# Kernel tuning notes

Measured on AMD Instinct MI355X. Metric: run time of the kernel, lower is better.

Reference implementation:

```python
import jax, jax.numpy as jnp
import numpy as np
import math

RES_SCALE = 1.0
NEG_INF = -1e20
NORM_EPS = 5e-5


def _conv(x, w, pad):
    return jax.lax.conv_general_dilated(
        x, w, window_strides=(1, 1), padding=((pad, pad), (pad, pad)),
        dimension_numbers=("NCHW", "OIHW", "NCHW"))


def _blockify(t, bH, bW, nH, nW):
    # [N,C,H,W] -> [N, block_size, n_blocks, C]  (matches torch Unfold with
    # kernel=(bH,bW), stride=(bH,bW) then reshape+permute(0,2,3,1))
    n, c, _, _ = t.shape
    t = t.reshape(n, c, nH, bH, nW, bW)
    t = t.transpose(0, 1, 3, 5, 2, 4)          # [N,C,bH,bW,nH,nW]
    t = t.reshape(n, c, bH * bW, nH * nW)
    return t.transpose(0, 2, 3, 1)             # [N, block, n_blk, C]


def _unblockify(t, bH, bW, nH, nW):
    # [N, block_size, n_blocks, C] -> [N,C,H,W] (torch Fold inverse)
    n, blk, nblk, c = t.shape
    t = t.transpose(0, 3, 1, 2)                # [N,C,block,n_blk]
    t = t.reshape(n, c, bH, bW, nH, nW)
    t = t.transpose(0, 1, 4, 2, 5, 3)          # [N,C,nH,bH,nW,bW]
    return t.reshape(n, c, nH * bH, nW * bW)


def setup_inputs() -> dict:
    key = jax.random.key(0)
    k1, k2, k3, k4, k5 = jax.random.split(key, 5)
    N, C, H, W = 8, 64, 256, 256
    Cq = C // 4  # reduction=4
    x = jax.random.normal(k1, (N, C, H, W), dtype=jnp.float32)
    w_match = jax.random.normal(k2, (Cq, C, 3, 3), dtype=jnp.float32) * (1.0 / math.sqrt(C * 9))
    b_match = jax.random.normal(k3, (Cq,), dtype=jnp.float32) * 0.01
    w_asm = jax.random.normal(k4, (C, C, 1, 1), dtype=jnp.float32) * (1.0 / math.sqrt(C))
    b_asm = jax.random.normal(k5, (C,), dtype=jnp.float32) * 0.01
    return {"x": x, "w_match": w_match, "b_match": b_match,
            "w_asm": w_asm, "b_asm": b_asm}


def reference(x, w_match, b_match, w_asm, b_asm):
    N, C, H, W = x.shape
    bH = math.ceil(math.sqrt(H)); nH = bH
    bW = math.ceil(math.sqrt(W)); nW = bW
    # H=W=256 -> bH=bW=16, perfect blocking, no padding needed.
    block_size = bH * bW
    n_blocks = nH * nW

    x_embed = _conv(x, w_match, pad=1) + b_match[None, :, None, None]   # [N,Cq,H,W]
    y_embed = _conv(x, w_asm, pad=0) + b_asm[None, :, None, None]       # [N,C,H,W]

    xq = _blockify(x_embed, bH, bW, nH, nW)   # [N, block, n_blk, Cq]
    yv = _blockify(y_embed, bH, bW, nH, nW)   # [N, block, n_blk, C]

    # F.normalize(p=2, dim=-1, eps=5e-5): x / max(||x||, eps)
    norm = jnp.sqrt(jnp.sum(xq * xq, axis=-1, keepdims=True))
    xk = xq / jnp.maximum(norm, NORM_EPS)

    # attention across blocks at fixed intra-block position
    raw = jnp.einsum("bkie,bkje->bkij", xq, xk)      # [N, block, n_blk, n_blk]
    diag = jnp.eye(n_blocks, dtype=bool)
    raw = jnp.where(diag[None, None], NEG_INF, raw)
    score = jax.nn.softmax(raw, axis=-1)             # exp(raw - logsumexp)

    ret = jnp.einsum("bkij,bkje->bkie", score, yv)   # [N, block, n_blk, C]
    ret = _unblockify(ret, bH, bW, nH, nW)           # [N,C,H,W]

    return ret * RES_SCALE + x
```

## Files before the change

kernel.cpp:

```cpp
#include <hip/hip_runtime.h>
#include <math.h>

typedef __attribute__((ext_vector_type(8))) short bf16x8;
typedef __attribute__((ext_vector_type(4))) float f32x4;

#define HH 256
#define WW 256
#define HW (HH*WW)
#define NORM_EPS 5e-5f

#define OFF_WASMT   0
#define OFF_WMATT   4096
#define OFF_RNORM   16384
#define OFF_QBLK    540672
#define OFF_VBLK    8929280

__global__ void k_transpose_w(const float* __restrict__ w_asm,
                              const float* __restrict__ w_match,
                              float* __restrict__ ws) {
    int t = threadIdx.x;
    float* wasmT = ws + OFF_WASMT;
    float* wmatT = ws + OFF_WMATT;
    for (int idx = t; idx < 64 * 64; idx += 256) {
        int ci = idx >> 6, c = idx & 63;
        wasmT[ci * 64 + c] = w_asm[c * 64 + ci];
    }
    for (int idx = t; idx < 576 * 16; idx += 256) {
        int e = idx & 15, r = idx >> 4;
        wmatT[idx] = w_match[e * 576 + r];
    }
}

__global__ __launch_bounds__(256) void k_conv1x1(const float* __restrict__ x,
                                                 const float* __restrict__ b_asm,
                                                 const float* __restrict__ ws_r,
                                                 float* __restrict__ vblk) {
    int p = blockIdx.x * 256 + threadIdx.x;
    int n = p >> 16;
    int h = (p >> 8) & 255;
    int w = p & 255;
    const float* wasmT = ws_r + OFF_WASMT;

    float acc[64];
#pragma unroll
    for (int c = 0; c < 64; ++c) acc[c] = b_asm[c];

    const float* xp = x + n * (64 * HW) + h * WW + w;
#pragma unroll 4
    for (int ci = 0; ci < 64; ++ci) {
        float xv = xp[ci * HW];
        const float* wr = wasmT + ci * 64;
#pragma unroll
        for (int c = 0; c < 64; ++c) acc[c] = fmaf(xv, wr[c], acc[c]);
    }

    int k = ((h & 15) << 4) | (w & 15);
    int j = ((h >> 4) << 4) | (w >> 4);
    float* out = vblk + (size_t)(((n << 8) | k) * 256 + j) * 64;
#pragma unroll
    for (int c4 = 0; c4 < 16; ++c4) {
        reinterpret_cast<float4*>(out)[c4] =
            make_float4(acc[c4 * 4], acc[c4 * 4 + 1], acc[c4 * 4 + 2], acc[c4 * 4 + 3]);
    }
}

__global__ __launch_bounds__(256) void k_conv3x3(const float* __restrict__ x,
                                                 const float* __restrict__ b_match,
                                                 const float* __restrict__ ws_r,
                                                 float* __restrict__ qblk,
                                                 float* __restrict__ rnorm) {
    int p = blockIdx.x * 256 + threadIdx.x;
    int n = p >> 16;
    int h = (p >> 8) & 255;
    int w = p & 255;
    const float* wmatT = ws_r + OFF_WMATT;

    float acc[16];
#pragma unroll
    for (int e = 0; e < 16; ++e) acc[e] = b_match[e];

    const float* xb = x + n * (64 * HW) + h * WW + w;
    bool hm = h > 0, hp = h < 255, wmk = w > 0, wpk = w < 255;

    for (int ci = 0; ci < 64; ++ci) {
        const float* xc = xb + ci * HW;
        float xv[9];
        xv[0] = (hm && wmk) ? xc[-WW - 1] : 0.f;
        xv[1] = hm          ? xc[-WW]     : 0.f;
        xv[2] = (hm && wpk) ? xc[-WW + 1] : 0.f;
        xv[3] = wmk         ? xc[-1]      : 0.f;
        xv[4] =               xc[0];
        xv[5] = wpk         ? xc[1]       : 0.f;
        xv[6] = (hp && wmk) ? xc[WW - 1]  : 0.f;
        xv[7] = hp          ? xc[WW]      : 0.f;
        xv[8] = (hp && wpk) ? xc[WW + 1]  : 0.f;
        const float* wr = wmatT + ci * 144;
#pragma unroll
        for (int t9 = 0; t9 < 9; ++t9) {
            float v = xv[t9];
#pragma unroll
            for (int e = 0; e < 16; ++e) acc[e] = fmaf(v, wr[t9 * 16 + e], acc[e]);
        }
    }

    float ss = 0.f;
#pragma unroll
    for (int e = 0; e < 16; ++e) ss = fmaf(acc[e], acc[e], ss);
    float rn = 1.0f / fmaxf(sqrtf(ss), NORM_EPS);

    int k = ((h & 15) << 4) | (w & 15);
    int j = ((h >> 4) << 4) | (w >> 4);
    size_t base = (size_t)(((n << 8) | k) * 256 + j);
    rnorm[base] = rn;
    float* out = qblk + base * 16;
#pragma unroll
    for (int e4 = 0; e4 < 4; ++e4) {
        reinterpret_cast<float4*>(out)[e4] =
            make_float4(acc[e4 * 4], acc[e4 * 4 + 1], acc[e4 * 4 + 2], acc[e4 * 4 + 3]);
    }
}

#define QP  0
#define KP  20480
#define VTH 40960
#define VTL 50176
#define PB  59392

#define MFMA16(A,B,C) __builtin_amdgcn_mfma_f32_16x16x32_bf16((A),(B),(C),0,0,0)

__global__ __launch_bounds__(256, 2) void k_attn(const float* __restrict__ ws_r,
                                                 float* __restrict__ vblk) {
    __shared__ __align__(16) unsigned char sm[64512];
    const int tid  = threadIdx.x;
    const int lane = tid & 63;
    const int wv   = tid >> 6;
    const int g    = lane >> 4;
    const int l15  = lane & 15;
    const bool hi32 = lane >= 32;
    const int b = blockIdx.x;

    const bf16x8 zfrag = {0,0,0,0,0,0,0,0};

    const float* qbase  = ws_r + OFF_QBLK  + (size_t)b * (256 * 16);
    const float* rnbase = ws_r + OFF_RNORM + (size_t)b * 256;
    float* vbase = vblk + (size_t)b * (256 * 64);

    {
        const int t = tid;
        float rn = rnbase[t];
        const float4* q4 = reinterpret_cast<const float4*>(qbase + t * 16);
        float q[16];
#pragma unroll
        for (int r = 0; r < 4; ++r) {
            float4 v = q4[r];
            q[4*r+0] = v.x; q[4*r+1] = v.y; q[4*r+2] = v.z; q[4*r+3] = v.w;
        }
        unsigned qh[8], ql[8], kh[8], kl[8];
#pragma unroll
        for (int e = 0; e < 8; ++e) {
            float a0 = q[2*e], a1 = q[2*e+1];
            unsigned u0 = __float_as_uint(a0) & 0xFFFF0000u;
            unsigned u1 = __float_as_uint(a1) & 0xFFFF0000u;
            float r0 = a0 - __uint_as_float(u0);
            float r1 = a1 - __uint_as_float(u1);
            qh[e] = (u0 >> 16) | u1;
            ql[e] = ((__float_as_uint(r0) & 0xFFFF0000u) >> 16) | (__float_as_uint(r1) & 0xFFFF0000u);
            float k0 = a0 * rn, k1 = a1 * rn;
            unsigned v0 = __float_as_uint(k0) & 0xFFFF0000u;
            unsigned v1 = __float_as_uint(k1) & 0xFFFF0000u;
            float s0 = k0 - __uint_as_float(v0);
            float s1 = k1 - __uint_as_float(v1);
            kh[e] = (v0 >> 16) | v1;
            kl[e] = ((__float_as_uint(s0) & 0xFFFF0000u) >> 16) | (__float_as_uint(s1) & 0xFFFF0000u);
        }
        uint4* qrow = reinterpret_cast<uint4*>(sm + QP + t * 80);
        qrow[0] = make_uint4(qh[0], qh[1], qh[2], qh[3]);
        qrow[1] = make_uint4(qh[4], qh[5], qh[6], qh[7]);
        qrow[2] = make_uint4(ql[0], ql[1], ql[2], ql[3]);
        qrow[3] = make_uint4(ql[4], ql[5], ql[6], ql[7]);
        uint4* krow = reinterpret_cast<uint4*>(sm + KP + t * 80);
        krow[0] = make_uint4(kh[0], kh[1], kh[2], kh[3]);
        krow[1] = make_uint4(kh[4], kh[5], kh[6], kh[7]);
        krow[2] = make_uint4(kl[0], kl[1], kl[2], kl[3]);
        krow[3] = make_uint4(kl[4], kl[5], kl[6], kl[7]);
    }
    __syncthreads();

    bf16x8 qb1[4], qb2[4];
#pragma unroll
    for (int it = 0; it < 4; ++it) {
        int i0 = wv * 64 + it * 16;
        qb1[it] = *reinterpret_cast<const bf16x8*>(sm + QP + (i0 + l15) * 80 + (g & 1) * 16);
        bf16x8 t2 = *reinterpret_cast<const bf16x8*>(sm + QP + (i0 + l15) * 80 + 32 + (g & 1) * 16);
        qb2[it] = hi32 ? zfrag : t2;
    }

    float mrow[4] = {-1e30f, -1e30f, -1e30f, -1e30f};
    for (int jt = 0; jt < 16; ++jt) {
        bf16x8 kf = *reinterpret_cast<const bf16x8*>(sm + KP + (jt * 16 + l15) * 80 + g * 16);
#pragma unroll
        for (int it = 0; it < 4; ++it) {
            f32x4 s = {0.f, 0.f, 0.f, 0.f};
            s = MFMA16(kf, qb1[it], s);
            s = MFMA16(kf, qb2[it], s);
            bool dtile = (jt * 16 == wv * 64 + it * 16);
#pragma unroll
            for (int r = 0; r < 4; ++r) {
                float v = s[r];
                if (dtile && (4 * g + r == l15)) v = -1e30f;
                mrow[it] = fmaxf(mrow[it], v);
            }
        }
    }
#pragma unroll
    for (int it = 0; it < 4; ++it) {
        float m = mrow[it];
        m = fmaxf(m, __shfl_xor(m, 16, 64));
        m = fmaxf(m, __shfl_xor(m, 32, 64));
        mrow[it] = m;
    }

    float lsum[4] = {0.f, 0.f, 0.f, 0.f};
    f32x4 acc[4][4];
#pragma unroll
    for (int it = 0; it < 4; ++it)
#pragma unroll
        for (int ct = 0; ct < 4; ++ct) acc[it][ct] = (f32x4){0.f, 0.f, 0.f, 0.f};

    for (int ch = 0; ch < 4; ++ch) {
        __syncthreads();
        {
            int c = tid >> 2, jq = tid & 3;
            const float* vg = vbase + (size_t)(ch * 64) * 64 + c;
#pragma unroll
            for (int s2 = 0; s2 < 8; ++s2) {
                int jl = jq * 16 + s2 * 2;
                float v0 = vg[(size_t)jl * 64];
                float v1 = vg[(size_t)(jl + 1) * 64];
                unsigned u0 = __float_as_uint(v0) & 0xFFFF0000u;
                unsigned u1 = __float_as_uint(v1) & 0xFFFF0000u;
                float r0 = v0 - __uint_as_float(u0);
                float r1 = v1 - __uint_as_float(u1);
                *reinterpret_cast<unsigned*>(sm + VTH + c * 144 + jl * 2) = (u0 >> 16) | u1;
                *reinterpret_cast<unsigned*>(sm + VTL + c * 144 + jl * 2) =
                    ((__float_as_uint(r0) & 0xFFFF0000u) >> 16) | (__float_as_uint(r1) & 0xFFFF0000u);
            }
        }
        __syncthreads();

#pragma unroll
        for (int jt = 0; jt < 4; ++jt) {
            int jg0 = ch * 64 + jt * 16;
            int jl0 = jt * 16;
            bf16x8 kf = *reinterpret_cast<const bf16x8*>(sm + KP + (jg0 + l15) * 80 + g * 16);
            bf16x8 vh[4], vl[4];
#pragma unroll
            for (int ct = 0; ct < 4; ++ct) {
                vh[ct] = *reinterpret_cast<const bf16x8*>(
                    sm + VTH + (ct * 16 + l15) * 144 + (jl0 + 8 * (g & 1)) * 2);
                bf16x8 t2 = *reinterpret_cast<const bf16x8*>(
                    sm + VTL + (ct * 16 + l15) * 144 + (jl0 + 8 * (g & 1)) * 2);
                vl[ct] = hi32 ? zfrag : t2;
            }
#pragma unroll
            for (int it = 0; it < 4; ++it) {
                f32x4 s = {0.f, 0.f, 0.f, 0.f};
                s = MFMA16(kf, qb1[it], s);
                s = MFMA16(kf, qb2[it], s);
                bool dtile = (jg0 == wv * 64 + it * 16);
                unsigned pd[4];
#pragma unroll
                for (int r = 0; r < 4; ++r) {
                    float p = __expf(s[r] - mrow[it]);
                    if (dtile && (4 * g + r == l15)) p = 0.f;
                    lsum[it] += p;
                    unsigned uh = __float_as_uint(p) & 0xFFFF0000u;
                    float lo = p - __uint_as_float(uh);
                    unsigned ul = __float_as_uint(lo) & 0xFFFF0000u;
                    pd[r] = (uh >> 16) | ul;
                }
                *reinterpret_cast<uint4*>(sm + PB + wv * 1280 + l15 * 80 + g * 16) =
                    make_uint4(pd[0], pd[1], pd[2], pd[3]);
                const uint4 d0 = *reinterpret_cast<const uint4*>(sm + PB + wv * 1280 + l15 * 80 + (g & 1) * 32);
                const uint4 d1 = *reinterpret_cast<const uint4*>(sm + PB + wv * 1280 + l15 * 80 + (g & 1) * 32 + 16);
                unsigned bw0, bw1, bw2, bw3;
                if (!hi32) {
                    bw0 = (d0.x & 0xFFFFu) | (d0.y << 16);
                    bw1 = (d0.z & 0xFFFFu) | (d0.w << 16);
                    bw2 = (d1.x & 0xFFFFu) | (d1.y << 16);
                    bw3 = (d1.z & 0xFFFFu) | (d1.w << 16);
                } else {
                    bw0 = (d0.x >> 16) | (d0.y & 0xFFFF0000u);
                    bw1 = (d0.z >> 16) | (d0.w & 0xFFFF0000u);
                    bw2 = (d1.x >> 16) | (d1.y & 0xFFFF0000u);
                    bw3 = (d1.z >> 16) | (d1.w & 0xFFFF0000u);
                }
                union { uint4 u; bf16x8 s8; } pb_u;
                pb_u.u = make_uint4(bw0, bw1, bw2, bw3);
                bf16x8 pb = pb_u.s8;
#pragma unroll
                for (int ct = 0; ct < 4; ++ct) {
                    acc[it][ct] = MFMA16(vh[ct], pb, acc[it][ct]);
                    acc[it][ct] = MFMA16(vl[ct], pb, acc[it][ct]);
                }
            }
        }
    }

#pragma unroll
    for (int it = 0; it < 4; ++it) {
        float l = lsum[it];
        l += __shfl_xor(l, 16, 64);
        l += __shfl_xor(l, 32, 64);
        lsum[it] = 1.0f / l;
    }

    __syncthreads();
    const int obase = VTH + wv * 4352;
#pragma unroll
    for (int it = 0; it < 4; ++it) {
#pragma unroll
        for (int ct = 0; ct < 4; ++ct) {
#pragma unroll
            for (int r = 0; r < 4; ++r) {
                int c = ct * 16 + 4 * g + r;
                *reinterpret_cast<float*>(sm + obase + l15 * 272 + c * 4) =
                    acc[it][ct][r] * lsum[it];
            }
        }
        int ir = lane >> 2, cq = lane & 3;
        float* orow = vbase + (size_t)(wv * 64 + it * 16 + ir) * 64 + cq * 16;
#pragma unroll
        for (int k4 = 0; k4 < 4; ++k4) {
            float4 ov = *reinterpret_cast<const float4*>(sm + obase + ir * 272 + cq * 64 + k4 * 16);
            reinterpret_cast<float4*>(orow)[k4] = ov;
        }
    }
}

__global__ __launch_bounds__(256) void k_unblock(const float* __restrict__ oblk,
                                                 const float* __restrict__ x,
                                                 float* __restrict__ out) {
    int b = blockIdx.x;
    int n = b >> 8, h = b & 255;
    int t = threadIdx.x;
    int c = t & 63, wq = t >> 6;
    int kh = h & 15, jh = h >> 4;

    const float* ob = oblk + ((size_t)n << 22);
    size_t xoff = (((size_t)(n * 64 + c)) << 16) + ((size_t)h << 8);
    const float4* xr   = reinterpret_cast<const float4*>(x + xoff);
    float4*       outr = reinterpret_cast<float4*>(out + xoff);

    for (int it = 0; it < 16; ++it) {
        int w4 = wq * 16 + it;
        int w0 = w4 * 4;
        float vals[4];
#pragma unroll
        for (int r = 0; r < 4; ++r) {
            int w = w0 + r;
            int wm = w & 15, wd = w >> 4;
            vals[r] = ob[(((size_t)(kh * 16 + wm)) << 14) + ((jh * 16 + wd) << 6) + c];
        }
        float4 xv = xr[w4];
        outr[w4] = make_float4(vals[0] + xv.x, vals[1] + xv.y, vals[2] + xv.z, vals[3] + xv.w);
    }
}

extern "C" void kernel_launch(void* const* d_in, const int* in_sizes, int n_in,
                              void* d_out, int out_size, void* d_ws, size_t ws_size,
                              hipStream_t stream) {
    const float* x       = (const float*)d_in[0];
    const float* w_match = (const float*)d_in[1];
    const float* b_match = (const float*)d_in[2];
    const float* w_asm   = (const float*)d_in[3];
    const float* b_asm   = (const float*)d_in[4];
    float* out = (float*)d_out;
    float* ws  = (float*)d_ws;

    k_transpose_w<<<1, 256, 0, stream>>>(w_asm, w_match, ws);
    k_conv1x1<<<2048, 256, 0, stream>>>(x, b_asm, ws, ws + OFF_VBLK);
    k_conv3x3<<<2048, 256, 0, stream>>>(x, b_match, ws, ws + OFF_QBLK, ws + OFF_RNORM);
    k_attn<<<2048, 256, 0, stream>>>(ws, ws + OFF_VBLK);
    k_unblock<<<2048, 256, 0, stream>>>(ws + OFF_VBLK, x, out);
}
```

Baseline: 704.1 us.

## Fuse 1x1 and 3x3 convs into one MFMA kernel with split-bf16 precision

Replaces the two scalar-FMA convolution kernels with a single fused kernel that stages three input rows, with halo, in shared memory as hi/lo bf16 pairs. Both convolutions then run as bf16 MFMA GEMMs, using three products (hh, lh, hl) to approximate fp32 accuracy. The goal is to cut the heavy scalar FMA cost and read x only once for both convs. The risks are precision loss from dropping the lo*lo term and scattered 4-byte global stores into the blocked layout.

```diff
diff --git a/kernel.cpp b/kernel.cpp
--- a/kernel.cpp
+++ b/kernel.cpp
@@ -9,114 +9,180 @@
 #define HW (HH*WW)
 #define NORM_EPS 5e-5f
 
-#define OFF_WASMT   0
-#define OFF_WMATT   4096
+#define MFMA16(A,B,C) __builtin_amdgcn_mfma_f32_16x16x32_bf16((A),(B),(C),0,0,0)
+
 #define OFF_RNORM   16384
 #define OFF_QBLK    540672
 #define OFF_VBLK    8929280
-
-__global__ void k_transpose_w(const float* __restrict__ w_asm,
-                              const float* __restrict__ w_match,
-                              float* __restrict__ ws) {
+#define WASMH_U 0
+#define WASML_U 4096
+#define WMATH_U 8192
+#define WMATL_U 17408
+
+__global__ void k_prep(const float* __restrict__ w_asm,
+                       const float* __restrict__ w_match,
+                       unsigned short* __restrict__ wsu) {
     int t = threadIdx.x;
-    float* wasmT = ws + OFF_WASMT;
-    float* wmatT = ws + OFF_WMATT;
-    for (int idx = t; idx < 64 * 64; idx += 256) {
-        int ci = idx >> 6, c = idx & 63;
-        wasmT[ci * 64 + c] = w_asm[c * 64 + ci];
-    }
-    for (int idx = t; idx < 576 * 16; idx += 256) {
-        int e = idx & 15, r = idx >> 4;
-        wmatT[idx] = w_match[e * 576 + r];
+    for (int i = t; i < 4096; i += 256) {
+        float v = w_asm[i];
+        unsigned hh = __float_as_uint(v) & 0xFFFF0000u;
+        float lo = v - __uint_as_float(hh);
+        wsu[WASMH_U + i] = (unsigned short)(hh >> 16);
+        wsu[WASML_U + i] = (unsigned short)(__float_as_uint(lo) >> 16);
+    }
+    for (int i = t; i < 9216; i += 256) {
+        int tap = i >> 10, cout = (i >> 6) & 15, ci = i & 63;
+        float v = w_match[(cout * 64 + ci) * 9 + tap];
+        unsigned hh = __float_as_uint(v) & 0xFFFF0000u;
+        float lo = v - __uint_as_float(hh);
+        wsu[WMATH_U + i] = (unsigned short)(hh >> 16);
+        wsu[WMATL_U + i] = (unsigned short)(__float_as_uint(lo) >> 16);
     }
 }
 
-__global__ __launch_bounds__(256) void k_conv1x1(const float* __restrict__ x,
-                                                 const float* __restrict__ b_asm,
-                                                 const float* __restrict__ ws_r,
-                                                 float* __restrict__ vblk) {
-    int p = blockIdx.x * 256 + threadIdx.x;
-    int n = p >> 16;
-    int h = (p >> 8) & 255;
-    int w = p & 255;
-    const float* wasmT = ws_r + OFF_WASMT;
-
-    float acc[64];
-#pragma unroll
-    for (int c = 0; c < 64; ++c) acc[c] = b_asm[c];
-
-    const float* xp = x + n * (64 * HW) + h * WW + w;
-#pragma unroll 4
-    for (int ci = 0; ci < 64; ++ci) {
-        float xv = xp[ci * HW];
-        const float* wr = wasmT + ci * 64;
-#pragma unroll
-        for (int c = 0; c < 64; ++c) acc[c] = fmaf(xv, wr[c], acc[c]);
-    }
-
-    int k = ((h & 15) << 4) | (w & 15);
-    int j = ((h >> 4) << 4) | (w >> 4);
-    float* out = vblk + (size_t)(((n << 8) | k) * 256 + j) * 64;
-#pragma unroll
-    for (int c4 = 0; c4 < 16; ++c4) {
-        reinterpret_cast<float4*>(out)[c4] =
-            make_float4(acc[c4 * 4], acc[c4 * 4 + 1], acc[c4 * 4 + 2], acc[c4 * 4 + 3]);
-    }
-}
-
-__global__ __launch_bounds__(256) void k_conv3x3(const float* __restrict__ x,
-                                                 const float* __restrict__ b_match,
-                                                 const float* __restrict__ ws_r,
-                                                 float* __restrict__ qblk,
-                                                 float* __restrict__ rnorm) {
-    int p = blockIdx.x * 256 + threadIdx.x;
-    int n = p >> 16;
-    int h = (p >> 8) & 255;
-    int w = p & 255;
-    const float* wmatT = ws_r + OFF_WMATT;
-
-    float acc[16];
-#pragma unroll
-    for (int e = 0; e < 16; ++e) acc[e] = b_match[e];
-
-    const float* xb = x + n * (64 * HW) + h * WW + w;
-    bool hm = h > 0, hp = h < 255, wmk = w > 0, wpk = w < 255;
-
-    for (int ci = 0; ci < 64; ++ci) {
-        const float* xc = xb + ci * HW;
-        float xv[9];
-        xv[0] = (hm && wmk) ? xc[-WW - 1] : 0.f;
-        xv[1] = hm          ? xc[-WW]     : 0.f;
-        xv[2] = (hm && wpk) ? xc[-WW + 1] : 0.f;
-        xv[3] = wmk         ? xc[-1]      : 0.f;
-        xv[4] =               xc[0];
-        xv[5] = wpk         ? xc[1]       : 0.f;
-        xv[6] = (hp && wmk) ? xc[WW - 1]  : 0.f;
-        xv[7] = hp          ? xc[WW]      : 0.f;
-        xv[8] = (hp && wpk) ? xc[WW + 1]  : 0.f;
-        const float* wr = wmatT + ci * 144;
-#pragma unroll
-        for (int t9 = 0; t9 < 9; ++t9) {
-            float v = xv[t9];
-#pragma unroll
-            for (int e = 0; e < 16; ++e) acc[e] = fmaf(v, wr[t9 * 16 + e], acc[e]);
-        }
-    }
-
-    float ss = 0.f;
-#pragma unroll
-    for (int e = 0; e < 16; ++e) ss = fmaf(acc[e], acc[e], ss);
-    float rn = 1.0f / fmaxf(sqrtf(ss), NORM_EPS);
-
-    int k = ((h & 15) << 4) | (w & 15);
-    int j = ((h >> 4) << 4) | (w >> 4);
-    size_t base = (size_t)(((n << 8) | k) * 256 + j);
-    rnorm[base] = rn;
-    float* out = qblk + base * 16;
-#pragma unroll
-    for (int e4 = 0; e4 < 4; ++e4) {
-        reinterpret_cast<float4*>(out)[e4] =
-            make_float4(acc[e4 * 4], acc[e4 * 4 + 1], acc[e4 * 4 + 2], acc[e4 * 4 + 3]);
+__global__ __launch_bounds__(256, 2) void k_convs(const float* __restrict__ x,
+                                                  const float* __restrict__ b_match,
+                                                  const float* __restrict__ b_asm,
+                                                  const unsigned short* __restrict__ wsu,
+                                                  float* __restrict__ qblk,
+                                                  float* __restrict__ rnorm,
+                                                  float* __restrict__ vblk) {
+    __shared__ __align__(16) unsigned char smx[57024];
+    const int XL = 28512;
+    const int b = blockIdx.x;
+    const int n = b >> 10, h = (b >> 2) & 255, wseg = b & 3;
+    const int ws0 = wseg * 64;
+    const int t = threadIdx.x;
+    const int wl = t & 63, cq = t >> 6;
+
+    const float* xb = x + (size_t)n * 64 * HW;
+
+    for (int r = 0; r < 3; ++r) {
+        int hr = h - 1 + r;
+        bool okh = (hr >= 0) && (hr < 256);
+        unsigned hh[8], ll[8];
+#pragma unroll
+        for (int i2 = 0; i2 < 8; ++i2) {
+            float v0 = 0.f, v1 = 0.f;
+            if (okh) {
+                int ci0 = cq * 16 + i2 * 2;
+                v0 = xb[(size_t)ci0 * HW + hr * 256 + ws0 + wl];
+                v1 = xb[(size_t)(ci0 + 1) * HW + hr * 256 + ws0 + wl];
+            }
+            unsigned u0 = __float_as_uint(v0) & 0xFFFF0000u;
+            unsigned u1 = __float_as_uint(v1) & 0xFFFF0000u;
+            float r0 = v0 - __uint_as_float(u0);
+            float r1 = v1 - __uint_as_float(u1);
+            hh[i2] = (u0 >> 16) | u1;
+            ll[i2] = ((__float_as_uint(r0) & 0xFFFF0000u) >> 16) | (__float_as_uint(r1) & 0xFFFF0000u);
+        }
+        int base = (r * 66 + wl + 1) * 144 + cq * 32;
+        *reinterpret_cast<uint4*>(smx + base)           = make_uint4(hh[0], hh[1], hh[2], hh[3]);
+        *reinterpret_cast<uint4*>(smx + base + 16)      = make_uint4(hh[4], hh[5], hh[6], hh[7]);
+        *reinterpret_cast<uint4*>(smx + XL + base)      = make_uint4(ll[0], ll[1], ll[2], ll[3]);
+        *reinterpret_cast<uint4*>(smx + XL + base + 16) = make_uint4(ll[4], ll[5], ll[6], ll[7]);
+    }
+    if (t < 192) {
+        int r = t >> 6, ci = t & 63;
+        int hr = h - 1 + r;
+        bool okh = (hr >= 0) && (hr < 256);
+        float e0 = 0.f, e1 = 0.f;
+        if (okh && ws0 > 0)   e0 = xb[(size_t)ci * HW + hr * 256 + ws0 - 1];
+        if (okh && ws0 < 192) e1 = xb[(size_t)ci * HW + hr * 256 + ws0 + 64];
+        unsigned u0 = __float_as_uint(e0) & 0xFFFF0000u;
+        float l0 = e0 - __uint_as_float(u0);
+        unsigned u1 = __float_as_uint(e1) & 0xFFFF0000u;
+        float l1 = e1 - __uint_as_float(u1);
+        *reinterpret_cast<unsigned short*>(smx + (r * 66 + 0) * 144 + ci * 2)       = (unsigned short)(u0 >> 16);
+        *reinterpret_cast<unsigned short*>(smx + XL + (r * 66 + 0) * 144 + ci * 2)  = (unsigned short)(__float_as_uint(l0) >> 16);
+        *reinterpret_cast<unsigned short*>(smx + (r * 66 + 65) * 144 + ci * 2)      = (unsigned short)(u1 >> 16);
+        *reinterpret_cast<unsigned short*>(smx + XL + (r * 66 + 65) * 144 + ci * 2) = (unsigned short)(__float_as_uint(l1) >> 16);
+    }
+    __syncthreads();
+
+    const int lane = t & 63;
+    const int wv = t >> 6;
+    const int g = lane >> 4, l15 = lane & 15;
+
+    f32x4 accV[4], accQ;
+    {
+        float bq = b_match[l15];
+        accQ = (f32x4){bq, bq, bq, bq};
+#pragma unroll
+        for (int nt = 0; nt < 4; ++nt) {
+            float bv = b_asm[nt * 16 + l15];
+            accV[nt] = (f32x4){bv, bv, bv, bv};
+        }
+    }
+
+    {
+        int ab = (66 + wv * 16 + l15 + 1) * 144 + g * 16;
+        bf16x8 Ah0 = *reinterpret_cast<const bf16x8*>(smx + ab);
+        bf16x8 Ah1 = *reinterpret_cast<const bf16x8*>(smx + ab + 64);
+        bf16x8 Al0 = *reinterpret_cast<const bf16x8*>(smx + XL + ab);
+        bf16x8 Al1 = *reinterpret_cast<const bf16x8*>(smx + XL + ab + 64);
+#pragma unroll
+        for (int nt = 0; nt < 4; ++nt) {
+            const unsigned short* bp = wsu + (nt * 16 + l15) * 64 + g * 8;
+            bf16x8 Bh0 = *reinterpret_cast<const bf16x8*>(bp + WASMH_U);
+            bf16x8 Bh1 = *reinterpret_cast<const bf16x8*>(bp + WASMH_U + 32);
+            bf16x8 Bl0 = *reinterpret_cast<const bf16x8*>(bp + WASML_U);
+            bf16x8 Bl1 = *reinterpret_cast<const bf16x8*>(bp + WASML_U + 32);
+            accV[nt] = MFMA16(Ah0, Bh0, accV[nt]);
+            accV[nt] = MFMA16(Ah1, Bh1, accV[nt]);
+            accV[nt] = MFMA16(Al0, Bh0, accV[nt]);
+            accV[nt] = MFMA16(Al1, Bh1, accV[nt]);
+            accV[nt] = MFMA16(Ah0, Bl0, accV[nt]);
+            accV[nt] = MFMA16(Ah1, Bl1, accV[nt]);
+        }
+    }
+#pragma unroll
+    for (int dy = 0; dy < 3; ++dy) {
+#pragma unroll
+        for (int dx = 0; dx < 3; ++dx) {
+            int tap = dy * 3 + dx;
+            int ab = (dy * 66 + wv * 16 + l15 + dx) * 144 + g * 16;
+            bf16x8 Ah0 = *reinterpret_cast<const bf16x8*>(smx + ab);
+            bf16x8 Ah1 = *reinterpret_cast<const bf16x8*>(smx + ab + 64);
+            bf16x8 Al0 = *reinterpret_cast<const bf16x8*>(smx + XL + ab);
+            bf16x8 Al1 = *reinterpret_cast<const bf16x8*>(smx + XL + ab + 64);
+            const unsigned short* bp = wsu + (tap * 16 + l15) * 64 + g * 8;
+            bf16x8 Bh0 = *reinterpret_cast<const bf16x8*>(bp + WMATH_U);
+            bf16x8 Bh1 = *reinterpret_cast<const bf16x8*>(bp + WMATH_U + 32);
+            bf16x8 Bl0 = *reinterpret_cast<const bf16x8*>(bp + WMATL_U);
+            bf16x8 Bl1 = *reinterpret_cast<const bf16x8*>(bp + WMATL_U + 32);
+            accQ = MFMA16(Ah0, Bh0, accQ);
+            accQ = MFMA16(Ah1, Bh1, accQ);
+            accQ = MFMA16(Al0, Bh0, accQ);
+            accQ = MFMA16(Al1, Bh1, accQ);
+            accQ = MFMA16(Ah0, Bl0, accQ);
+            accQ = MFMA16(Ah1, Bl1, accQ);
+        }
+    }
+
+    const int khi = (h & 15) << 4;
+    const int j = ((h >> 4) << 4) | (wseg * 4 + wv);
+#pragma unroll
+    for (int r = 0; r < 4; ++r) {
+        float v = accQ[r];
+        float ss = v * v;
+        ss += __shfl_xor(ss, 1, 64);
+        ss += __shfl_xor(ss, 2, 64);
+        ss += __shfl_xor(ss, 4, 64);
+        ss += __shfl_xor(ss, 8, 64);
+        int m = 4 * g + r;
+        size_t rowbase = ((size_t)(n * 256 + (khi | m))) * 256 + j;
+        qblk[rowbase * 16 + l15] = v;
+        if (l15 == 0) rnorm[rowbase] = 1.0f / fmaxf(sqrtf(ss), NORM_EPS);
+    }
+#pragma unroll
+    for (int nt = 0; nt < 4; ++nt) {
+#pragma unroll
+        for (int r = 0; r < 4; ++r) {
+            int m = 4 * g + r;
+            size_t rowbase = ((size_t)(n * 256 + (khi | m))) * 256 + j;
+            vblk[rowbase * 64 + nt * 16 + l15] = accV[nt][r];
+        }
     }
 }
 
@@ -125,8 +191,6 @@
 #define VTH 40960
 #define VTL 50176
 #define PB  59392
-
-#define MFMA16(A,B,C) __builtin_amdgcn_mfma_f32_16x16x32_bf16((A),(B),(C),0,0,0)
 
 __global__ __launch_bounds__(256, 2) void k_attn(const float* __restrict__ ws_r,
                                                  float* __restrict__ vblk) {
@@ -378,9 +442,9 @@
     float* out = (float*)d_out;
     float* ws  = (float*)d_ws;
 
-    k_transpose_w<<<1, 256, 0, stream>>>(w_asm, w_match, ws);
-    k_conv1x1<<<2048, 256, 0, stream>>>(x, b_asm, ws, ws + OFF_VBLK);
-    k_conv3x3<<<2048, 256, 0, stream>>>(x, b_match, ws, ws + OFF_QBLK, ws + OFF_RNORM);
+    k_prep<<<1, 256, 0, stream>>>(w_asm, w_match, (unsigned short*)d_ws);
+    k_convs<<<8192, 256, 0, stream>>>(x, b_match, b_asm, (const unsigned short*)d_ws,
+                                      ws + OFF_QBLK, ws + OFF_RNORM, ws + OFF_VBLK);
     k_attn<<<2048, 256, 0, stream>>>(ws, ws + OFF_VBLK);
     k_unblock<<<2048, 256, 0, stream>>>(ws + OFF_VBLK, x, out);
 }
```

Result: slower. 718.4 us (+2.0%).
